# Performance work log

Hardware: AMD Instinct MI355X
Metric: run time of the kernel (lower is better)

## Reference

```python
import jax, jax.numpy as jnp
import numpy as np

B, S, F, H, T_OUT = 2048, 512, 32, 128, 24


def setup_inputs() -> dict:
    key = jax.random.key(0)
    ks = jax.random.split(key, 16)
    sc = 0.1
    return {
        "xb": jax.random.normal(ks[0], (B, S, F), dtype=jnp.float32),
        "enc_Wih": sc * jax.random.normal(ks[1], (3 * H, F), dtype=jnp.float32),
        "enc_Whh": sc * jax.random.normal(ks[2], (3 * H, H), dtype=jnp.float32),
        "enc_bih": sc * jax.random.normal(ks[3], (3 * H,), dtype=jnp.float32),
        "enc_bhh": sc * jax.random.normal(ks[4], (3 * H,), dtype=jnp.float32),
        "attn_W": sc * jax.random.normal(ks[5], (S, H + F), dtype=jnp.float32),
        "attn_b": sc * jax.random.normal(ks[6], (S,), dtype=jnp.float32),
        "dec_Wih": sc * jax.random.normal(ks[7], (3 * H, H), dtype=jnp.float32),
        "dec_Whh": sc * jax.random.normal(ks[8], (3 * H, H), dtype=jnp.float32),
        "dec_bih": sc * jax.random.normal(ks[9], (3 * H,), dtype=jnp.float32),
        "dec_bhh": sc * jax.random.normal(ks[10], (3 * H,), dtype=jnp.float32),
        "out1_W": sc * jax.random.normal(ks[11], (F, H), dtype=jnp.float32),
        "out1_b": sc * jax.random.normal(ks[12], (F,), dtype=jnp.float32),
        "out2_W": sc * jax.random.normal(ks[13], (1, F), dtype=jnp.float32),
        "out2_b": sc * jax.random.normal(ks[14], (1,), dtype=jnp.float32),
    }


def _gru_cell(x_proj, h, Whh, bhh):
    # x_proj: [B, 3H] = x @ Wih.T + bih (precomputed); torch GRU gate order r,z,n
    g_h = h @ Whh.T + bhh
    ir, iz, inn = jnp.split(x_proj, 3, axis=1)
    hr, hz, hn = jnp.split(g_h, 3, axis=1)
    r = jax.nn.sigmoid(ir + hr)
    z = jax.nn.sigmoid(iz + hz)
    n = jnp.tanh(inn + r * hn)
    return (1.0 - z) * n + z * h


def reference(xb, enc_Wih, enc_Whh, enc_bih, enc_bhh, attn_W, attn_b,
              dec_Wih, dec_Whh, dec_bih, dec_bhh, out1_W, out1_b, out2_W, out2_b):
    b = xb.shape[0]
    # ---- Encoder GRU (1 layer, unidirectional) ----
    x_proj = jnp.einsum('btf,gf->btg', xb, enc_Wih) + enc_bih  # [B,S,3H]

    def enc_step(h, xp):
        h = _gru_cell(xp, h, enc_Whh, enc_bhh)
        return h, h

    h0 = jnp.zeros((b, enc_Whh.shape[1]), dtype=xb.dtype)
    enc_hidden, enc_out = jax.lax.scan(enc_step, h0, jnp.swapaxes(x_proj, 0, 1))
    enc_out = jnp.swapaxes(enc_out, 0, 1)  # [B,S,H]

    # ---- Attention decoder loop ----
    y0 = xb[:, -1, :]  # [B,F]

    def dec_step(carry, _):
        h, y = carry
        ai = jnp.concatenate([h, y], axis=1)              # [B,H+F]
        w = jax.nn.softmax(ai @ attn_W.T + attn_b, axis=1)  # [B,S]
        ctx = jnp.einsum('bs,bsh->bh', w, enc_out)        # [B,H]
        xp = ctx @ dec_Wih.T + dec_bih
        h_new = _gru_cell(xp, h, dec_Whh, dec_bhh)
        out = h_new @ out1_W.T + out1_b                   # [B,F]
        return (h_new, out), out

    _, outs = jax.lax.scan(dec_step, (enc_hidden, y0), None, length=T_OUT)
    outs = jnp.swapaxes(outs, 0, 1)                       # [B,T_OUT,F]
    outs = jax.nn.relu(outs)
    outs = outs @ out2_W.T + out2_b                       # [B,T_OUT,1]
    outs = jax.nn.relu(outs)
    return outs.squeeze(-1)                               # [B,T_OUT]
```

## Files before the change

kernel.cpp:

```cpp
#include <hip/hip_runtime.h>
#include <hip/hip_fp16.h>

#define BB 2048
#define SS 512
#define FF 32
#define HH 128
#define TO 24
#define LOG2E 1.4426950408889634f

typedef unsigned int uint;
using half4 = __attribute__((ext_vector_type(4))) _Float16;
using half8 = __attribute__((ext_vector_type(8))) _Float16;
using f32x4 = __attribute__((ext_vector_type(4))) float;

#define OFF_ENCOUT 0ull
#define OFF_HFIN  (OFF_ENCOUT + (size_t)BB*SS*HH*2)
#define OFF_ATTNF (OFF_HFIN + (size_t)BB*HH*4)
#define OFF_ATTNB (OFF_ATTNF + (size_t)65536*2)
#define OFF_DECF  (OFF_ATTNB + (size_t)512*4)
#define OFF_OUT1F (OFF_DECF + (size_t)98304*2)
#define OFF_WF    (OFF_OUT1F + (size_t)4096*2)

__global__ void prep_kernel(const float* attn_W, const float* attn_b,
                            const float* dec_Wih, const float* dec_Whh,
                            const float* out1_W, const float* out1_b,
                            const float* enc_Wih, const float* enc_Whh,
                            __half* attnF, float* attnB, __half* decF, __half* out1F, __half* Wf) {
  int i = blockIdx.x * 256 + threadIdx.x;
  if (i < 65536) {
    int e = i & 7, l = (i >> 3) & 63, kb = (i >> 9) & 3, st = (i >> 11) & 3, w = i >> 13;
    int h = kb*32 + ((l >> 4) << 3) + e;
    int s = w*64 + st*16 + (l & 15);
    float acc = attn_W[s*160 + h];
    #pragma unroll 8
    for (int f = 0; f < 32; ++f) acc += out1_W[f*128 + h] * attn_W[s*160 + 128 + f];
    attnF[i] = __float2half(acc);
    return;
  }
  i -= 65536;
  if (i < 512) {
    float acc = attn_b[i];
    #pragma unroll 8
    for (int f = 0; f < 32; ++f) acc += out1_b[f] * attn_W[i*160 + 128 + f];
    attnB[i] = acc;
    return;
  }
  i -= 512;
  if (i < 98304) {
    int e = i & 7, l = (i >> 3) & 63, fi = (i >> 9) % 48, w = i / 24576;
    int lq = l >> 4, l15 = l & 15;
    float val;
    if (fi < 32) {
      int g2 = fi >> 4, sub = (fi >> 3) & 1, kb = fi & 7;
      int k = kb*32 + lq*8 + e, j = w*32 + sub*16 + l15, jg = g2*128 + j;
      val = (k < 128) ? dec_Wih[jg*128 + k] : dec_Whh[jg*128 + (k - 128)];
    } else {
      int f2 = fi - 32, cat = f2 >> 3, sub = (f2 >> 2) & 1, kb4 = f2 & 3;
      int k = kb4*32 + lq*8 + e, j = 256 + w*32 + sub*16 + l15;
      val = cat ? dec_Wih[j*128 + k] : dec_Whh[j*128 + k];
    }
    decF[i] = __float2half(val);
    return;
  }
  i -= 98304;
  if (i < 4096) {
    int e = i & 7, l = (i >> 3) & 63, kb = (i >> 9) & 3, tile = (i >> 11) & 1;
    int k = kb*32 + ((l >> 4) << 3) + e;
    int f = tile*16 + (l & 15);
    out1F[i] = __float2half(out1_W[f*128 + k]);
    return;
  }
  i -= 4096;
  if (i < 61440) {
    int e = i & 7, l = (i >> 3) & 63, q = i >> 9;
    int kb = q % 5, tt = (q / 5) % 6, w = q / 30;
    int g = tt >> 1, sub = tt & 1;
    int k = kb*32 + ((l >> 4) << 3) + e;
    int J = g*128 + w*32 + sub*16 + (l & 15);
    float v = (k < 128) ? enc_Whh[J*128 + k] : enc_Wih[J*32 + (k - 128)];
    Wf[i] = __float2half(v);
  }
}

#define HXS 168

__global__ void __launch_bounds__(256, 1) enc_kernel(
    const float* __restrict__ xb, const __half* __restrict__ Wf,
    const float* __restrict__ bih, const float* __restrict__ bhh,
    __half* __restrict__ enc_out, float* __restrict__ hfin) {
  __shared__ __align__(16) _Float16 hx[2][16][HXS];
  const int tid  = threadIdx.x;
  const int lane = tid & 63, wid = tid >> 6;
  const int l15  = lane & 15, lq = lane >> 4;
  const int b0   = blockIdx.x * 8;

  half8 Bf[6][5];
  { const half8* wfp = (const half8*)Wf;
    #pragma unroll
    for (int tt = 0; tt < 6; ++tt)
      #pragma unroll
      for (int kb = 0; kb < 5; ++kb)
        Bf[tt][kb] = wfp[((wid*6 + tt)*5 + kb)*64 + lane];
  }

  float br[2], bz[2], bnh[2], bni[2];
  #pragma unroll
  for (int sub = 0; sub < 2; ++sub) {
    int j = wid*32 + sub*16 + l15;
    br[sub]  = bih[j]       + bhh[j];
    bz[sub]  = bih[128 + j] + bhh[128 + j];
    bnh[sub] = bhh[256 + j];
    bni[sub] = bih[256 + j];
  }
  float hreg[2][4] = {{0.f,0.f,0.f,0.f},{0.f,0.f,0.f,0.f}};

  const int m2 = tid >> 5, c2 = tid & 31;

  for (int i = tid; i < 2*16*HXS; i += 256) (&hx[0][0][0])[i] = (_Float16)0.f;
  __syncthreads();
  hx[0][m2][128 + c2] = (_Float16)xb[((size_t)(b0 + m2)*512 + 0)*32 + c2];
  __syncthreads();

  int p = 0;
  for (int t = 0; t < 512; ++t) {
    const int tn = (t < 511) ? t + 1 : 511;
    float xpre = xb[((size_t)(b0 + m2)*512 + tn)*32 + c2];

    half8 A[5];
    #pragma unroll
    for (int kb = 0; kb < 5; ++kb)
      A[kb] = *(const half8*)&hx[p][l15][kb*32 + lq*8];

    f32x4 Cr[2], Cz[2], Cnh[2], Cni[2];
    #pragma unroll
    for (int sub = 0; sub < 2; ++sub) {
      Cr[sub] = (f32x4){0.f,0.f,0.f,0.f};
      Cz[sub] = (f32x4){0.f,0.f,0.f,0.f};
      Cnh[sub] = (f32x4){0.f,0.f,0.f,0.f};
      Cni[sub] = (f32x4){0.f,0.f,0.f,0.f};
    }
    #pragma unroll
    for (int sub = 0; sub < 2; ++sub) {
      #pragma unroll
      for (int kb = 0; kb < 5; ++kb) {
        Cr[sub] = __builtin_amdgcn_mfma_f32_16x16x32_f16(A[kb], Bf[sub][kb],     Cr[sub], 0, 0, 0);
        Cz[sub] = __builtin_amdgcn_mfma_f32_16x16x32_f16(A[kb], Bf[2 + sub][kb], Cz[sub], 0, 0, 0);
      }
      #pragma unroll
      for (int kb = 0; kb < 4; ++kb)
        Cnh[sub] = __builtin_amdgcn_mfma_f32_16x16x32_f16(A[kb], Bf[4 + sub][kb], Cnh[sub], 0, 0, 0);
      Cni[sub] = __builtin_amdgcn_mfma_f32_16x16x32_f16(A[4], Bf[4 + sub][4], Cni[sub], 0, 0, 0);
    }

    #pragma unroll
    for (int sub = 0; sub < 2; ++sub)
      #pragma unroll
      for (int i = 0; i < 4; ++i) {
        float xr = Cr[sub][i] + br[sub];
        float xz = Cz[sub][i] + bz[sub];
        float r = __builtin_amdgcn_rcpf(1.f + __builtin_amdgcn_exp2f(-LOG2E*xr));
        float z = __builtin_amdgcn_rcpf(1.f + __builtin_amdgcn_exp2f(-LOG2E*xz));
        float narg = (Cni[sub][i] + bni[sub]) + r * (Cnh[sub][i] + bnh[sub]);
        float n = 1.f - 2.f*__builtin_amdgcn_rcpf(__builtin_amdgcn_exp2f((2.f*LOG2E)*narg) + 1.f);
        float hnew = n + z*(hreg[sub][i] - n);
        hreg[sub][i] = hnew;
        if (lq < 2)
          hx[p ^ 1][4*lq + i][wid*32 + sub*16 + l15] = (_Float16)hnew;
      }
    hx[p ^ 1][m2][128 + c2] = (_Float16)xpre;
    __syncthreads();

    { half4 hv = *(const half4*)&hx[p ^ 1][m2][c2*4];
      *(half4*)((void*)&enc_out[((size_t)(b0 + m2)*512 + t)*128 + c2*4]) = hv; }
    p ^= 1;
  }

  if (lq < 2)
    #pragma unroll
    for (int sub = 0; sub < 2; ++sub)
      #pragma unroll
      for (int i = 0; i < 4; ++i)
        hfin[(size_t)(b0 + 4*lq + i)*128 + wid*32 + sub*16 + l15] = hreg[sub][i];
}

struct DecSmem {
  _Float16 ET[128*512];
  _Float16 wsm[512];
  float hsm[128];
  _Float16 hh[128];
  _Float16 cxh[2][256];
  _Float16 hist[TO*128];
  float red[16];
  float d32[32];
};

__global__ void __launch_bounds__(512, 2) dec_kernel(const float* __restrict__ xb,
    const __half* __restrict__ enc_out, const float* __restrict__ hfin,
    const __half* __restrict__ attnF, const float* __restrict__ attnB,
    const float* __restrict__ attn_W,
    const __half* __restrict__ decF, const __half* __restrict__ out1F,
    const float* __restrict__ dbih, const float* __restrict__ dbhh,
    const float* __restrict__ out1_W, const float* __restrict__ out1_b,
    const float* __restrict__ out2_W, const float* __restrict__ out2_b,
    float* __restrict__ out) {
  __shared__ __align__(16) DecSmem sm;
  const int tid = threadIdx.x, lane = tid & 63, wid = tid >> 6;
  const int l15 = lane & 15, lq = lane >> 4;
  const int b = blockIdx.x;

  const half8* aFp = (const half8*)attnF;
  const half8* dFp = (const half8*)decF;
  const half8* oFp = (const half8*)out1F;
  const int Wb = wid >> 1, sb = wid & 1;

  const float ab = attnB[tid];
  const int jg = wid*16 + l15;
  const float bR  = dbih[jg]       + dbhh[jg];
  const float bZ  = dbih[128 + jg] + dbhh[128 + jg];
  const float bNH = dbhh[256 + jg];
  const float bNI = dbih[256 + jg];
  const float o1b0 = out1_b[l15], o1b1 = out1_b[16 + l15];
  const float o2w0 = out2_W[l15], o2w1 = out2_W[16 + l15];
  const float o2b  = out2_b[0];

  { const half8* src = (const half8*)(enc_out + (size_t)b*512*128);
    for (int i = tid; i < 8192; i += 512) {
      half8 v = src[i];
      int s = i >> 4, h0 = (i & 15) * 8, sg = s >> 3, s7 = s & 7;
      #pragma unroll
      for (int j = 0; j < 8; ++j) {
        int h = h0 + j;
        sm.ET[h*512 + (((sg ^ (h & 7) ^ ((h >> 3) & 7)) << 3)) + s7] = v[j];
      }
    } }
  if (tid < 128) { float hv = hfin[(size_t)b*128 + tid];
    sm.hsm[tid] = hv; sm.hh[tid] = (_Float16)hv; sm.cxh[0][128 + tid] = (_Float16)hv; }
  if (tid < 32) {
    float o1v = out1_b[tid];
    for (int h = 0; h < 128; ++h) o1v += out1_W[tid*128 + h] * hfin[(size_t)b*128 + h];
    sm.d32[tid] = xb[((size_t)b*512 + 511)*32 + tid] - o1v;
  }
  __syncthreads();
  float c0reg = 0.f;
  #pragma unroll 8
  for (int f = 0; f < 32; ++f) c0reg += sm.d32[f] * attn_W[tid*160 + 128 + f];

  const half8 Az = {};
  const int hrow = wid*16 + l15;
  const int hswz = (hrow & 7) ^ ((hrow >> 3) & 7);

  for (int tt = 0; tt < TO; ++tt) {
    _Float16* cxhR = sm.cxh[tt & 1];
    _Float16* cxhW = sm.cxh[(tt & 1) ^ 1];

    half8 A[4];
    #pragma unroll
    for (int kb = 0; kb < 4; ++kb)
      A[kb] = (l15 == 0) ? *(const half8*)&sm.hh[kb*32 + lq*8] : Az;
    f32x4 CL[4];
    #pragma unroll
    for (int stt = 0; stt < 4; ++stt) CL[stt] = (f32x4){0.f,0.f,0.f,0.f};
    #pragma unroll
    for (int stt = 0; stt < 4; ++stt)
      #pragma unroll
      for (int kb = 0; kb < 4; ++kb)
        CL[stt] = __builtin_amdgcn_mfma_f32_16x16x32_f16(
            A[kb], aFp[((wid*4 + stt)*4 + kb)*64 + lane], CL[stt], 0, 0, 0);
    float t0 = __shfl(CL[0][0], l15), t1 = __shfl(CL[1][0], l15);
    float t2 = __shfl(CL[2][0], l15), t3 = __shfl(CL[3][0], l15);
    float v = (lq == 0) ? t0 : (lq == 1) ? t1 : (lq == 2) ? t2 : t3;
    v += ab;
    if (tt == 0) v += c0reg;
    float mw = v;
    #pragma unroll
    for (int off = 1; off < 64; off <<= 1) mw = fmaxf(mw, __shfl_xor(mw, off));
    float sw = __builtin_amdgcn_exp2f(LOG2E*(v - mw));
    #pragma unroll
    for (int off = 1; off < 64; off <<= 1) sw += __shfl_xor(sw, off);
    if (lane == 0) { sm.red[wid] = mw; sm.red[8 + wid] = sw; }
    __syncthreads();

    float M = sm.red[0];
    #pragma unroll
    for (int g = 1; g < 8; ++g) M = fmaxf(M, sm.red[g]);
    float tot = 0.f;
    #pragma unroll
    for (int g = 0; g < 8; ++g) tot += sm.red[8 + g] * __builtin_amdgcn_exp2f(LOG2E*(sm.red[g] - M));
    float wv = __builtin_amdgcn_exp2f(LOG2E*(v - M)) * __builtin_amdgcn_rcpf(tot);
    sm.wsm[tid] = (_Float16)wv;
    __syncthreads();

    f32x4 Ca[2];
    Ca[0] = (f32x4){0.f,0.f,0.f,0.f}; Ca[1] = (f32x4){0.f,0.f,0.f,0.f};
    #pragma unroll
    for (int kb = 0; kb < 16; ++kb) {
      const half8 bet = *(const half8*)&sm.ET[hrow*512 + (((kb*4 + lq) ^ hswz) << 3)];
      const half8 aw  = (l15 == 0) ? *(const half8*)&sm.wsm[kb*32 + lq*8] : Az;
      Ca[kb & 1] = __builtin_amdgcn_mfma_f32_16x16x32_f16(aw, bet, Ca[kb & 1], 0, 0, 0);
    }
    if (lane < 16)
      cxhR[wid*16 + l15] = (_Float16)(Ca[0][0] + Ca[1][0]);
    __syncthreads();

    half8 Ag[8];
    #pragma unroll
    for (int kb = 0; kb < 8; ++kb)
      Ag[kb] = (l15 == 0) ? *(const half8*)&cxhR[kb*32 + lq*8] : Az;
    f32x4 Cr, Cz, Cnh4, Cni4;
    Cr = (f32x4){0.f,0.f,0.f,0.f}; Cz = (f32x4){0.f,0.f,0.f,0.f};
    Cnh4 = (f32x4){0.f,0.f,0.f,0.f}; Cni4 = (f32x4){0.f,0.f,0.f,0.f};
    #pragma unroll
    for (int kb = 0; kb < 8; ++kb) {
      Cr = __builtin_amdgcn_mfma_f32_16x16x32_f16(Ag[kb], dFp[(Wb*48 +      sb*8 + kb)*64 + lane], Cr, 0, 0, 0);
      Cz = __builtin_amdgcn_mfma_f32_16x16x32_f16(Ag[kb], dFp[(Wb*48 + 16 + sb*8 + kb)*64 + lane], Cz, 0, 0, 0);
    }
    #pragma unroll
    for (int kb = 0; kb < 4; ++kb) {
      Cnh4 = __builtin_amdgcn_mfma_f32_16x16x32_f16(Ag[4 + kb], dFp[(Wb*48 + 32 + sb*4 + kb)*64 + lane], Cnh4, 0, 0, 0);
      Cni4 = __builtin_amdgcn_mfma_f32_16x16x32_f16(Ag[kb],     dFp[(Wb*48 + 40 + sb*4 + kb)*64 + lane], Cni4, 0, 0, 0);
    }
    if (lane < 16) {
      float xr = Cr[0] + bR, xz = Cz[0] + bZ;
      float r = __builtin_amdgcn_rcpf(1.f + __builtin_amdgcn_exp2f(-LOG2E*xr));
      float z = __builtin_amdgcn_rcpf(1.f + __builtin_amdgcn_exp2f(-LOG2E*xz));
      float narg = (Cni4[0] + bNI) + r * (Cnh4[0] + bNH);
      float n = 1.f - 2.f*__builtin_amdgcn_rcpf(__builtin_amdgcn_exp2f((2.f*LOG2E)*narg) + 1.f);
      float hnew = n + z*(sm.hsm[jg] - n);
      sm.hsm[jg] = hnew;
      _Float16 hf = (_Float16)hnew;
      sm.hh[jg] = hf;
      cxhW[128 + jg] = hf;
      sm.hist[tt*128 + jg] = hf;
    }
    __syncthreads();
  }

  if (wid == 0) {
    #pragma unroll
    for (int chunk = 0; chunk < 2; ++chunk) {
      half8 Ae[4];
      #pragma unroll
      for (int kb = 0; kb < 4; ++kb) {
        int step = chunk*16 + l15;
        Ae[kb] = (step < TO) ? *(const half8*)&sm.hist[step*128 + kb*32 + lq*8] : Az;
      }
      f32x4 C0, C1;
      C0 = (f32x4){0.f,0.f,0.f,0.f}; C1 = (f32x4){0.f,0.f,0.f,0.f};
      #pragma unroll
      for (int kb = 0; kb < 4; ++kb) {
        C0 = __builtin_amdgcn_mfma_f32_16x16x32_f16(Ae[kb], oFp[kb*64 + lane],       C0, 0, 0, 0);
        C1 = __builtin_amdgcn_mfma_f32_16x16x32_f16(Ae[kb], oFp[(4 + kb)*64 + lane], C1, 0, 0, 0);
      }
      #pragma unroll
      for (int i = 0; i < 4; ++i) {
        int row = lq*4 + i, step = chunk*16 + row;
        float y0 = C0[i] + o1b0, y1 = C1[i] + o1b1;
        float part = fmaxf(y0, 0.f)*o2w0 + fmaxf(y1, 0.f)*o2w1;
        #pragma unroll
        for (int off = 1; off < 16; off <<= 1) part += __shfl_xor(part, off, 16);
        if (l15 == 0 && step < TO)
          out[(size_t)b*TO + step] = fmaxf(part + o2b, 0.f);
      }
    }
  }
}

extern "C" void kernel_launch(void* const* d_in, const int* in_sizes, int n_in,
                              void* d_out, int out_size, void* d_ws, size_t ws_size,
                              hipStream_t stream) {
  const float* xb      = (const float*)d_in[0];
  const float* enc_Wih = (const float*)d_in[1];
  const float* enc_Whh = (const float*)d_in[2];
  const float* enc_bih = (const float*)d_in[3];
  const float* enc_bhh = (const float*)d_in[4];
  const float* attn_W  = (const float*)d_in[5];
  const float* attn_b  = (const float*)d_in[6];
  const float* dec_Wih = (const float*)d_in[7];
  const float* dec_Whh = (const float*)d_in[8];
  const float* dec_bih = (const float*)d_in[9];
  const float* dec_bhh = (const float*)d_in[10];
  const float* out1_W  = (const float*)d_in[11];
  const float* out1_b  = (const float*)d_in[12];
  const float* out2_W  = (const float*)d_in[13];
  const float* out2_b  = (const float*)d_in[14];

  char* ws = (char*)d_ws;
  __half* enc_out = (__half*)(ws + OFF_ENCOUT);
  float*  hfin    = (float*)(ws + OFF_HFIN);
  __half* attnF   = (__half*)(ws + OFF_ATTNF);
  float*  attnB   = (float*)(ws + OFF_ATTNB);
  __half* decF    = (__half*)(ws + OFF_DECF);
  __half* out1F   = (__half*)(ws + OFF_OUT1F);
  __half* Wf      = (__half*)(ws + OFF_WF);

  prep_kernel<<<900, 256, 0, stream>>>(attn_W, attn_b, dec_Wih, dec_Whh, out1_W, out1_b,
                                       enc_Wih, enc_Whh, attnF, attnB, decF, out1F, Wf);
  enc_kernel<<<256, 256, 0, stream>>>(xb, Wf, enc_bih, enc_bhh, enc_out, hfin);
  dec_kernel<<<2048, 512, 0, stream>>>(xb, enc_out, hfin, attnF, attnB, attn_W, decF, out1F,
                                       dec_bih, dec_bhh, out1_W, out1_b, out2_W, out2_b,
                                       (float*)d_out);
}
```

Baseline: 1.106 ms.

## Split encoder GRU across 8 waves per block and prefetch decoder weight fragments

The encoder block grows from 4 to 8 waves, so each wave handles 16 hidden columns instead of 32. This halves the serial MFMA chain and gate math per wave on each of the 512 recurrent steps, and the enc_out store is redistributed across all waves. In the decoder, the GRU weight fragments are loaded into registers at the top of each step instead of inline in the MFMA calls, which lets the global loads overlap the attention phase. The costs are more threads syncing per step in the encoder and higher register pressure in the decoder, which runs two 512-thread blocks per CU.

```diff
diff --git a/kernel.cpp b/kernel.cpp
--- a/kernel.cpp
+++ b/kernel.cpp
@@ -9,6 +9,7 @@
 #define LOG2E 1.4426950408889634f
 
 typedef unsigned int uint;
+using half2v = __attribute__((ext_vector_type(2))) _Float16;
 using half4 = __attribute__((ext_vector_type(4))) _Float16;
 using half8 = __attribute__((ext_vector_type(8))) _Float16;
 using f32x4 = __attribute__((ext_vector_type(4))) float;
@@ -84,7 +85,7 @@
 
 #define HXS 168
 
-__global__ void __launch_bounds__(256, 1) enc_kernel(
+__global__ void __launch_bounds__(512, 1) enc_kernel(
     const float* __restrict__ xb, const __half* __restrict__ Wf,
     const float* __restrict__ bih, const float* __restrict__ bhh,
     __half* __restrict__ enc_out, float* __restrict__ hfin) {
@@ -93,94 +94,79 @@
   const int lane = tid & 63, wid = tid >> 6;
   const int l15  = lane & 15, lq = lane >> 4;
   const int b0   = blockIdx.x * 8;
-
-  half8 Bf[6][5];
+  const int ow   = wid >> 1, sub = wid & 1;
+  const int j    = wid*16 + l15;
+
+  half8 Bfr[5], Bfz[5], Bfn[5];
   { const half8* wfp = (const half8*)Wf;
     #pragma unroll
-    for (int tt = 0; tt < 6; ++tt)
-      #pragma unroll
-      for (int kb = 0; kb < 5; ++kb)
-        Bf[tt][kb] = wfp[((wid*6 + tt)*5 + kb)*64 + lane];
-  }
-
-  float br[2], bz[2], bnh[2], bni[2];
-  #pragma unroll
-  for (int sub = 0; sub < 2; ++sub) {
-    int j = wid*32 + sub*16 + l15;
-    br[sub]  = bih[j]       + bhh[j];
-    bz[sub]  = bih[128 + j] + bhh[128 + j];
-    bnh[sub] = bhh[256 + j];
-    bni[sub] = bih[256 + j];
-  }
-  float hreg[2][4] = {{0.f,0.f,0.f,0.f},{0.f,0.f,0.f,0.f}};
-
-  const int m2 = tid >> 5, c2 = tid & 31;
-
-  for (int i = tid; i < 2*16*HXS; i += 256) (&hx[0][0][0])[i] = (_Float16)0.f;
+    for (int kb = 0; kb < 5; ++kb) {
+      Bfr[kb] = wfp[((ow*6 + sub)*5     + kb)*64 + lane];
+      Bfz[kb] = wfp[((ow*6 + 2 + sub)*5 + kb)*64 + lane];
+      Bfn[kb] = wfp[((ow*6 + 4 + sub)*5 + kb)*64 + lane];
+    }
+  }
+  const float br  = bih[j]       + bhh[j];
+  const float bz  = bih[128 + j] + bhh[128 + j];
+  const float bnh = bhh[256 + j];
+  const float bni = bih[256 + j];
+  float hreg[4] = {0.f, 0.f, 0.f, 0.f};
+
+  const int m2 = (tid >> 5) & 7, c2 = tid & 31;
+
+  for (int i = tid; i < 2*16*HXS; i += 512) (&hx[0][0][0])[i] = (_Float16)0.f;
   __syncthreads();
-  hx[0][m2][128 + c2] = (_Float16)xb[((size_t)(b0 + m2)*512 + 0)*32 + c2];
+  if (tid < 256) hx[0][m2][128 + c2] = (_Float16)xb[((size_t)(b0 + m2)*512 + 0)*32 + c2];
   __syncthreads();
 
   int p = 0;
   for (int t = 0; t < 512; ++t) {
     const int tn = (t < 511) ? t + 1 : 511;
-    float xpre = xb[((size_t)(b0 + m2)*512 + tn)*32 + c2];
+    float xpre = 0.f;
+    if (tid < 256) xpre = xb[((size_t)(b0 + m2)*512 + tn)*32 + c2];
 
     half8 A[5];
     #pragma unroll
     for (int kb = 0; kb < 5; ++kb)
       A[kb] = *(const half8*)&hx[p][l15][kb*32 + lq*8];
 
-    f32x4 Cr[2], Cz[2], Cnh[2], Cni[2];
-    #pragma unroll
-    for (int sub = 0; sub < 2; ++sub) {
-      Cr[sub] = (f32x4){0.f,0.f,0.f,0.f};
-      Cz[sub] = (f32x4){0.f,0.f,0.f,0.f};
-      Cnh[sub] = (f32x4){0.f,0.f,0.f,0.f};
-      Cni[sub] = (f32x4){0.f,0.f,0.f,0.f};
-    }
-    #pragma unroll
-    for (int sub = 0; sub < 2; ++sub) {
-      #pragma unroll
-      for (int kb = 0; kb < 5; ++kb) {
-        Cr[sub] = __builtin_amdgcn_mfma_f32_16x16x32_f16(A[kb], Bf[sub][kb],     Cr[sub], 0, 0, 0);
-        Cz[sub] = __builtin_amdgcn_mfma_f32_16x16x32_f16(A[kb], Bf[2 + sub][kb], Cz[sub], 0, 0, 0);
-      }
-      #pragma unroll
-      for (int kb = 0; kb < 4; ++kb)
-        Cnh[sub] = __builtin_amdgcn_mfma_f32_16x16x32_f16(A[kb], Bf[4 + sub][kb], Cnh[sub], 0, 0, 0);
-      Cni[sub] = __builtin_amdgcn_mfma_f32_16x16x32_f16(A[4], Bf[4 + sub][4], Cni[sub], 0, 0, 0);
-    }
-
-    #pragma unroll
-    for (int sub = 0; sub < 2; ++sub)
-      #pragma unroll
-      for (int i = 0; i < 4; ++i) {
-        float xr = Cr[sub][i] + br[sub];
-        float xz = Cz[sub][i] + bz[sub];
-        float r = __builtin_amdgcn_rcpf(1.f + __builtin_amdgcn_exp2f(-LOG2E*xr));
-        float z = __builtin_amdgcn_rcpf(1.f + __builtin_amdgcn_exp2f(-LOG2E*xz));
-        float narg = (Cni[sub][i] + bni[sub]) + r * (Cnh[sub][i] + bnh[sub]);
-        float n = 1.f - 2.f*__builtin_amdgcn_rcpf(__builtin_amdgcn_exp2f((2.f*LOG2E)*narg) + 1.f);
-        float hnew = n + z*(hreg[sub][i] - n);
-        hreg[sub][i] = hnew;
-        if (lq < 2)
-          hx[p ^ 1][4*lq + i][wid*32 + sub*16 + l15] = (_Float16)hnew;
-      }
-    hx[p ^ 1][m2][128 + c2] = (_Float16)xpre;
+    f32x4 Cr = {0.f,0.f,0.f,0.f}, Cz = {0.f,0.f,0.f,0.f};
+    f32x4 Cnh = {0.f,0.f,0.f,0.f}, Cni = {0.f,0.f,0.f,0.f};
+    #pragma unroll
+    for (int kb = 0; kb < 5; ++kb) {
+      Cr = __builtin_amdgcn_mfma_f32_16x16x32_f16(A[kb], Bfr[kb], Cr, 0, 0, 0);
+      Cz = __builtin_amdgcn_mfma_f32_16x16x32_f16(A[kb], Bfz[kb], Cz, 0, 0, 0);
+    }
+    #pragma unroll
+    for (int kb = 0; kb < 4; ++kb)
+      Cnh = __builtin_amdgcn_mfma_f32_16x16x32_f16(A[kb], Bfn[kb], Cnh, 0, 0, 0);
+    Cni = __builtin_amdgcn_mfma_f32_16x16x32_f16(A[4], Bfn[4], Cni, 0, 0, 0);
+
+    #pragma unroll
+    for (int i = 0; i < 4; ++i) {
+      float xr = Cr[i] + br;
+      float xz = Cz[i] + bz;
+      float r = __builtin_amdgcn_rcpf(1.f + __builtin_amdgcn_exp2f(-LOG2E*xr));
+      float z = __builtin_amdgcn_rcpf(1.f + __builtin_amdgcn_exp2f(-LOG2E*xz));
+      float narg = (Cni[i] + bni) + r * (Cnh[i] + bnh);
+      float n = 1.f - 2.f*__builtin_amdgcn_rcpf(__builtin_amdgcn_exp2f((2.f*LOG2E)*narg) + 1.f);
+      float hnew = n + z*(hreg[i] - n);
+      hreg[i] = hnew;
+      if (lq < 2)
+        hx[p ^ 1][4*lq + i][j] = (_Float16)hnew;
+    }
+    if (tid < 256) hx[p ^ 1][m2][128 + c2] = (_Float16)xpre;
     __syncthreads();
 
-    { half4 hv = *(const half4*)&hx[p ^ 1][m2][c2*4];
-      *(half4*)((void*)&enc_out[((size_t)(b0 + m2)*512 + t)*128 + c2*4]) = hv; }
+    { half2v hv = *(const half2v*)&hx[p ^ 1][wid][lane*2];
+      *(half2v*)((void*)&enc_out[((size_t)(b0 + wid)*512 + t)*128 + lane*2]) = hv; }
     p ^= 1;
   }
 
   if (lq < 2)
     #pragma unroll
-    for (int sub = 0; sub < 2; ++sub)
-      #pragma unroll
-      for (int i = 0; i < 4; ++i)
-        hfin[(size_t)(b0 + 4*lq + i)*128 + wid*32 + sub*16 + l15] = hreg[sub][i];
+    for (int i = 0; i < 4; ++i)
+      hfin[(size_t)(b0 + 4*lq + i)*128 + j] = hreg[i];
 }
 
 struct DecSmem {
@@ -253,6 +239,18 @@
     _Float16* cxhR = sm.cxh[tt & 1];
     _Float16* cxhW = sm.cxh[(tt & 1) ^ 1];
 
+    half8 BrzR[8], BrzZ[8], Bnh4[4], Bni4[4];
+    #pragma unroll
+    for (int kb = 0; kb < 8; ++kb) {
+      BrzR[kb] = dFp[(Wb*48 +      sb*8 + kb)*64 + lane];
+      BrzZ[kb] = dFp[(Wb*48 + 16 + sb*8 + kb)*64 + lane];
+    }
+    #pragma unroll
+    for (int kb = 0; kb < 4; ++kb) {
+      Bnh4[kb] = dFp[(Wb*48 + 32 + sb*4 + kb)*64 + lane];
+      Bni4[kb] = dFp[(Wb*48 + 40 + sb*4 + kb)*64 + lane];
+    }
+
     half8 A[4];
     #pragma unroll
     for (int kb = 0; kb < 4; ++kb)
@@ -311,13 +309,13 @@
     Cnh4 = (f32x4){0.f,0.f,0.f,0.f}; Cni4 = (f32x4){0.f,0.f,0.f,0.f};
     #pragma unroll
     for (int kb = 0; kb < 8; ++kb) {
-      Cr = __builtin_amdgcn_mfma_f32_16x16x32_f16(Ag[kb], dFp[(Wb*48 +      sb*8 + kb)*64 + lane], Cr, 0, 0, 0);
-      Cz = __builtin_amdgcn_mfma_f32_16x16x32_f16(Ag[kb], dFp[(Wb*48 + 16 + sb*8 + kb)*64 + lane], Cz, 0, 0, 0);
+      Cr = __builtin_amdgcn_mfma_f32_16x16x32_f16(Ag[kb], BrzR[kb], Cr, 0, 0, 0);
+      Cz = __builtin_amdgcn_mfma_f32_16x16x32_f16(Ag[kb], BrzZ[kb], Cz, 0, 0, 0);
     }
     #pragma unroll
     for (int kb = 0; kb < 4; ++kb) {
-      Cnh4 = __builtin_amdgcn_mfma_f32_16x16x32_f16(Ag[4 + kb], dFp[(Wb*48 + 32 + sb*4 + kb)*64 + lane], Cnh4, 0, 0, 0);
-      Cni4 = __builtin_amdgcn_mfma_f32_16x16x32_f16(Ag[kb],     dFp[(Wb*48 + 40 + sb*4 + kb)*64 + lane], Cni4, 0, 0, 0);
+      Cnh4 = __builtin_amdgcn_mfma_f32_16x16x32_f16(Ag[4 + kb], Bnh4[kb], Cnh4, 0, 0, 0);
+      Cni4 = __builtin_amdgcn_mfma_f32_16x16x32_f16(Ag[kb],     Bni4[kb], Cni4, 0, 0, 0);
     }
     if (lane < 16) {
       float xr = Cr[0] + bR, xz = Cz[0] + bZ;
@@ -395,7 +393,7 @@
 
   prep_kernel<<<900, 256, 0, stream>>>(attn_W, attn_b, dec_Wih, dec_Whh, out1_W, out1_b,
                                        enc_Wih, enc_Whh, attnF, attnB, decF, out1F, Wf);
-  enc_kernel<<<256, 256, 0, stream>>>(xb, Wf, enc_bih, enc_bhh, enc_out, hfin);
+  enc_kernel<<<256, 512, 0, stream>>>(xb, Wf, enc_bih, enc_bhh, enc_out, hfin);
   dec_kernel<<<2048, 512, 0, stream>>>(xb, enc_out, hfin, attnF, attnB, attn_W, decF, out1F,
                                        dec_bih, dec_bhh, out1_W, out1_b, out2_W, out2_b,
                                        (float*)d_out);
```

New measurement: 1.166 ms. 1.05x slower.
